# Kernel optimization log

Hardware: AMD Instinct MI355X
Metric: run time of the kernel (lower is better)

## Reference

```python
import jax, jax.numpy as jnp
import numpy as np
import math

NUM_HEADS = 8
HEAD_DIM = 32  # num_units 256 / 8 heads
TIME_DIM = 8
NEG_BIG = -2.0 ** 32 + 1.0


def _ffn(x, W1, b1, W2, b2):
    # two-layer relu MLP: 1 -> time_dim -> time_dim
    h = jax.nn.relu(x @ W1 + b1)
    return jax.nn.relu(h @ W2 + b2)


def _time_gsm_kernel(t, pW1, pb1, pW2, pb2, sW1, sb1, sW2, sb2, bW1, bb1, bW2, bb2):
    # t: [B, L] timestamps -> kernel [B, L, L]
    tt = t[..., None]  # [B, L, 1]
    period = _ffn(tt, pW1, pb1, pW2, pb2)        # [B, L, td]
    qpq = (2.0 * math.pi) * period * tt           # [B, L, td]
    period_diff = qpq[:, :, None, :] - qpq[:, None, :, :]  # [B, Lq, Lk, td]
    cos_enc = jnp.cos(period_diff)
    sigma = _ffn(tt, sW1, sb1, sW2, sb2)          # [B, L, td]
    sq = sigma[:, :, None, :] + 1e-6              # [B, Lq, 1, td] bcast
    sk = sigma[:, None, :, :] + 1e-6              # [B, 1, Lk, td] bcast
    denom = sq ** 2 + sk ** 2
    t_diff = t[:, :, None] - t[:, None, :]        # [B, Lq, Lk]
    exp_enc = jnp.exp(-(t_diff[..., None] ** 2) / denom)
    local_enc = jnp.sqrt(2.0 * sq * sk / denom)
    basis = _ffn(tt, bW1, bb1, bW2, bb2)          # [B, L, td]
    basis_qk = basis[:, :, None, :] * basis[:, None, :, :]
    return jnp.sum(basis_qk * local_enc * exp_enc * cos_enc, axis=-1)  # [B, L, L]


def setup_inputs() -> dict:
    key = jax.random.key(0)
    ks = jax.random.split(key, 20)
    B, L, U = 4, 1024, 256
    td = TIME_DIM
    inp = {
        'query_input': jax.random.normal(ks[0], (B, L, U), dtype=jnp.float32),
        'input_tensor': jax.random.normal(ks[1], (B, L, U), dtype=jnp.float32),
        'input_mask': jnp.ones((B, L), dtype=jnp.int32),
        'time_inputs': jax.random.uniform(ks[2], (B, L), dtype=jnp.float32) * 100.0,
        'att_bias': jnp.zeros((1,), dtype=jnp.int32),
        'Wq': jax.random.normal(ks[3], (U, U), dtype=jnp.float32) * 0.05,
        'Wk': jax.random.normal(ks[4], (U, U), dtype=jnp.float32) * 0.05,
        'Wv': jax.random.normal(ks[5], (U, U), dtype=jnp.float32) * 0.05,
    }
    names = ['p', 's', 'b']
    i = 6
    for n in names:
        inp[n + 'W1'] = jax.random.normal(ks[i], (1, td), dtype=jnp.float32) * 0.5; i += 1
        inp[n + 'b1'] = jnp.zeros((td,), dtype=jnp.float32)
        inp[n + 'W2'] = jax.random.normal(ks[i], (td, td), dtype=jnp.float32) * 0.5; i += 1
        inp[n + 'b2'] = jnp.zeros((td,), dtype=jnp.float32)
    return inp


def reference(query_input, input_tensor, input_mask, time_inputs, att_bias,
              Wq, Wk, Wv,
              pW1, pb1, pW2, pb2, sW1, sb1, sW2, sb2, bW1, bb1, bW2, bb2):
    B, Lq, U = query_input.shape
    Lk = input_tensor.shape[1]
    H, dh = NUM_HEADS, HEAD_DIM

    Q = (query_input @ Wq).reshape(B, Lq, H, dh).transpose(0, 2, 1, 3)  # [B,H,Lq,dh]
    K = (input_tensor @ Wk).reshape(B, Lk, H, dh).transpose(0, 2, 1, 3)
    V = (input_tensor @ Wv).reshape(B, Lk, H, dh).transpose(0, 2, 1, 3)

    scale = 1.0 / math.sqrt(dh)
    scores = jnp.einsum('bhqd,bhkd->bhqk', Q, K) * scale  # [B,H,Lq,Lk]

    tk = _time_gsm_kernel(time_inputs, pW1, pb1, pW2, pb2,
                          sW1, sb1, sW2, sb2, bW1, bb1, bW2, bb2)  # [B,Lq,Lk]
    scores = scores + tk[:, None, :, :] * scale

    # key padding mask: zero-norm keys get -inf-like score
    key_masks = jnp.sign(jnp.sum(jnp.abs(K), axis=-1))  # [B,H,Lk]
    scores = jnp.where(key_masks[:, :, None, :] == 0.0, NEG_BIG, scores)

    # direction == 'forward': allow strictly row > col (strict causal)
    idx = jnp.arange(Lk)
    causal = (idx[:, None] > idx[None, :]).astype(scores.dtype)  # [Lq,Lk]
    scores = scores + (1.0 - causal) * -10000.0

    attn = jax.nn.softmax(scores, axis=-1)

    query_masks = jnp.sign(jnp.sum(jnp.abs(Q), axis=-1))  # [B,H,Lq]
    attn = attn * query_masks[..., None]
    # dropout rate 0.0 -> identity

    out = jnp.einsum('bhqk,bhkd->bhqd', attn, V)
    out = out.transpose(0, 2, 1, 3).reshape(B, Lq, U)
    out = out * input_mask.astype(jnp.float32)[..., None]
    return out
```

## Files before the change

### kernel.cpp

```cpp
#include <hip/hip_runtime.h>
#include <math.h>

#define B_DIM 4
#define L_DIM 1024
#define H_DIM 8
#define D_DIM 32
#define TD 8
#define NTILES_TOT 1056
#define SCALE 0.17677669529663687f

typedef unsigned short ushort_t;
typedef __attribute__((ext_vector_type(8))) short short8v;
typedef __attribute__((ext_vector_type(4))) float f32x4;

__device__ __forceinline__ int ntiles_of(int qt) { return (qt >> 1) + 1; }
__device__ __forceinline__ int off_of(int qt) {
  int m = qt >> 1;
  return (qt & 1) ? (m + 1) * (m + 1) : m * m + m;
}
__device__ __forceinline__ void qcseg(int x, int& qc, int& s) {
  if (x < 4) { qc = x; s = 0; }
  else if (x < 12) { qc = 4 + ((x - 4) >> 1); s = (x - 4) & 1; }
  else if (x < 24) { int t = x - 12; qc = 8 + t / 3; s = t % 3; }
  else { int t = x - 24; qc = 12 + (t >> 2); s = t & 3; }
}

__device__ __forceinline__ ushort_t f2bf(float f) {
  unsigned u = __builtin_bit_cast(unsigned, f);
  u += 0x7FFFu + ((u >> 16) & 1u);
  return (ushort_t)(u >> 16);
}
__device__ __forceinline__ float bf2f(ushort_t h) {
  return __builtin_bit_cast(float, ((unsigned)h) << 16);
}
__device__ __forceinline__ short8v pack84(float4 a, float4 b) {
  short8v r;
  r[0] = (short)f2bf(a.x); r[1] = (short)f2bf(a.y);
  r[2] = (short)f2bf(a.z); r[3] = (short)f2bf(a.w);
  r[4] = (short)f2bf(b.x); r[5] = (short)f2bf(b.y);
  r[6] = (short)f2bf(b.z); r[7] = (short)f2bf(b.w);
  return r;
}

__global__ __launch_bounds__(256) void prep_kernel(
    const float* __restrict__ t_in,
    const float* __restrict__ pW1, const float* __restrict__ pb1,
    const float* __restrict__ pW2, const float* __restrict__ pb2,
    const float* __restrict__ sW1, const float* __restrict__ sb1,
    const float* __restrict__ sW2, const float* __restrict__ sb2,
    const float* __restrict__ bW1, const float* __restrict__ bb1,
    const float* __restrict__ bW2, const float* __restrict__ bb2,
    float* __restrict__ ptf, float* __restrict__ sg, float* __restrict__ bs,
    const float* __restrict__ Xq, const float* __restrict__ Xi,
    ushort_t* __restrict__ Xfq, ushort_t* __restrict__ Xfi,
    const float* __restrict__ Wq, const float* __restrict__ Wk,
    const float* __restrict__ Wv, ushort_t* __restrict__ Wf) {
  const int blk = blockIdx.x;
  const int tid = threadIdx.x;
  if (blk < 512) {
    const int lin = blk * 256 + tid;
    const int i = lin >> 5;
    const int slot = lin & 31;
    const int z = slot >> 3, e = slot & 7;
    if (z == 3) return;
    const float* W1 = (z == 0) ? pW1 : (z == 1) ? sW1 : bW1;
    const float* b1 = (z == 0) ? pb1 : (z == 1) ? sb1 : bb1;
    const float* W2 = (z == 0) ? pW2 : (z == 1) ? sW2 : bW2;
    const float* b2 = (z == 0) ? pb2 : (z == 1) ? sb2 : bb2;
    const double t = (double)t_in[i];
    double acc = (double)b2[e];
#pragma unroll
    for (int d = 0; d < 8; ++d) {
      double hv = t * (double)W1[d] + (double)b1[d];
      hv = hv > 0.0 ? hv : 0.0;
      acc += hv * (double)W2[d * 8 + e];
    }
    acc = acc > 0.0 ? acc : 0.0;
    const size_t o = (size_t)i * TD + e;
    if (z == 0) {
      double pt = acc * t;
      ptf[o] = (float)(pt - floor(pt));
    } else if (z == 1) {
      sg[o] = (float)(acc + 1e-6);
    } else {
      bs[o] = (float)acc;
    }
  } else if (blk < 1536) {
    const int xb = blk - 512;
    const float* X = (xb < 512) ? Xq : Xi;
    ushort_t* O = (xb < 512) ? Xfq : Xfi;
    const int lin = (xb & 511) * 256 + tid;
    const int row = lin >> 5, q = lin & 31;
    const float* src = &X[(size_t)row * 256 + q * 8];
    short8v f = pack84(*(const float4*)src, *(const float4*)(src + 4));
    size_t idx = ((size_t)((row >> 4) * 8 + (q >> 2)) * 64 + (q & 3) * 16 + (row & 15)) * 8;
    *(short8v*)&O[idx] = f;
  } else {
    const int wb = blk - 1536;
    const int z = wb >> 5;
    const float* W = (z == 0) ? Wq : (z == 1) ? Wk : Wv;
    const int lin = (wb & 31) * 256 + tid;
    const int kt = lin >> 10, g = (lin >> 8) & 3, n = lin & 255;
    short8v f;
#pragma unroll
    for (int i2 = 0; i2 < 8; ++i2)
      f[i2] = (short)f2bf(W[(size_t)(kt * 32 + g * 8 + i2) * 256 + n]);
    size_t idx = ((size_t)((z * 8 + kt) * 16 + (n >> 4)) * 64 + g * 16 + (n & 15)) * 8;
    *(short8v*)&Wf[idx] = f;
  }
}

__global__ __launch_bounds__(256) void work_kernel(
    const ushort_t* __restrict__ Xfq, const ushort_t* __restrict__ Xfi,
    const ushort_t* __restrict__ Wf,
    ushort_t* __restrict__ Qf, ushort_t* __restrict__ Kf,
    ushort_t* __restrict__ Vf,
    const float* __restrict__ ptf, const float* __restrict__ sg,
    const float* __restrict__ bs, const float* __restrict__ t_in,
    float* __restrict__ tkbuf) {
  __shared__ __align__(16) float ptq[16 * 8], qsh[16 * 8], qbh[16 * 8];
  __shared__ __align__(16) float ptk[32 * 12], ksh[32 * 12], kbh[32 * 12];
  __shared__ float trow[16], tcol[32];
  const int blk = blockIdx.x;
  const int tid = threadIdx.x;

  if (blk < 384) {
    const int z = blk >> 7;
    const int rem = blk & 127;
    const int m0t = (rem & 31) * 8;
    const int n0 = (rem >> 5) * 64;
    const ushort_t* Xf = (z == 0) ? Xfq : Xfi;
    const int w = tid >> 6, l = tid & 63, lg = l >> 4, lc = l & 15;
    const int wm = w >> 1, wn = w & 1;

    f32x4 acc[4][2];
#pragma unroll
    for (int mi = 0; mi < 4; ++mi)
#pragma unroll
      for (int ni = 0; ni < 2; ++ni) acc[mi][ni] = (f32x4){0.f, 0.f, 0.f, 0.f};

    for (int kt0 = 0; kt0 < 8; ++kt0) {
      short8v a[4], bfr[2];
#pragma unroll
      for (int mi = 0; mi < 4; ++mi)
        a[mi] = *(const short8v*)&Xf[((size_t)(m0t + wm * 4 + mi) * 8 + kt0) * 512 + l * 8];
#pragma unroll
      for (int ni = 0; ni < 2; ++ni)
        bfr[ni] = *(const short8v*)&Wf[((size_t)(z * 8 + kt0) * 16 + (n0 >> 4) + wn * 2 + ni) * 512 + l * 8];
#pragma unroll
      for (int mi = 0; mi < 4; ++mi)
#pragma unroll
        for (int ni = 0; ni < 2; ++ni)
          acc[mi][ni] = __builtin_amdgcn_mfma_f32_16x16x32_bf16(a[mi], bfr[ni], acc[mi][ni], 0, 0, 0);
    }

#pragma unroll
    for (int mi = 0; mi < 4; ++mi) {
#pragma unroll
      for (int ni = 0; ni < 2; ++ni) {
        const int col = n0 + wn * 32 + ni * 16 + lc;
        const int hh = col >> 5, d = col & 31;
#pragma unroll
        for (int r = 0; r < 4; ++r) {
          const int row = (m0t + wm * 4 + mi) * 16 + lg * 4 + r;
          const int bb = row >> 10, lr = row & (L_DIM - 1);
          float v = acc[mi][ni][r];
          if (z == 0) v *= SCALE;
          const ushort_t bv = f2bf(v);
          if (z == 2) {
            Vf[(((size_t)(bb * H_DIM + hh) * 32 + (lr >> 5)) * 2 + (d >> 4)) * 512 +
               (((lr >> 3) & 3) * 16 + (d & 15)) * 8 + (lr & 7)] = bv;
          } else {
            ushort_t* of16 = (z == 0) ? Qf : Kf;
            of16[((size_t)((bb * H_DIM + hh) * 64 + (lr >> 4))) * 512 +
                 ((d >> 3) * 16 + (lr & 15)) * 8 + (d & 7)] = bv;
          }
        }
      }
    }
  } else {
    const int lin = blk - 384;
    const int b = lin / NTILES_TOT;
    const int t1 = lin - b * NTILES_TOT;
    int m = (int)sqrtf((float)t1 + 1.0f);
    while (m * m + m > t1) --m;
    while ((m + 1) * (m + 1) + (m + 1) <= t1) ++m;
    const int rem = t1 - (m * m + m);
    int qt, kt;
    if (rem <= m) { qt = 2 * m; kt = rem; }
    else          { qt = 2 * m + 1; kt = rem - (m + 1); }
    const int q0 = qt << 4, k0 = kt << 5;

    if (tid < 16) trow[tid] = t_in[b * L_DIM + q0 + tid];
    if (tid < 32) tcol[tid] = t_in[b * L_DIM + k0 + tid];
    if (tid < 128) {
      const int i = tid >> 3, d = tid & 7;
      const size_t base = (size_t)(b * L_DIM + q0 + i) * TD + d;
      ptq[i * 8 + d] = ptf[base];
      qsh[i * 8 + d] = sg[base];
      qbh[i * 8 + d] = bs[base];
    }
    {
      const int j = tid >> 3, d = tid & 7;
      const size_t base = (size_t)(b * L_DIM + k0 + j) * TD + d;
      ptk[j * 12 + d] = ptf[base];
      ksh[j * 12 + d] = sg[base];
      kbh[j * 12 + d] = bs[base];
    }
    __syncthreads();

    const int r = tid & 3;
    const int lr2 = tid >> 2;
    const int i = ((lr2 >> 4) << 2) | r;
    float pq[8], qs_[8], qb_[8];
    *(float4*)&pq[0]  = *(const float4*)&ptq[i * 8];
    *(float4*)&pq[4]  = *(const float4*)&ptq[i * 8 + 4];
    *(float4*)&qs_[0] = *(const float4*)&qsh[i * 8];
    *(float4*)&qs_[4] = *(const float4*)&qsh[i * 8 + 4];
    *(float4*)&qb_[0] = *(const float4*)&qbh[i * 8];
    *(float4*)&qb_[4] = *(const float4*)&qbh[i * 8 + 4];
    const float ti = trow[i];

    float* dst = &tkbuf[(size_t)(b * NTILES_TOT + off_of(qt) + kt) * 512];
#pragma unroll
    for (int pp = 0; pp < 2; ++pp) {
      const int j = pp * 16 + (lr2 & 15);
      float td2 = ti - tcol[j];
      td2 *= td2;
      float pk[8], ks_[8], kb_[8];
      *(float4*)&pk[0]  = *(const float4*)&ptk[j * 12];
      *(float4*)&pk[4]  = *(const float4*)&ptk[j * 12 + 4];
      *(float4*)&ks_[0] = *(const float4*)&ksh[j * 12];
      *(float4*)&ks_[4] = *(const float4*)&ksh[j * 12 + 4];
      *(float4*)&kb_[0] = *(const float4*)&kbh[j * 12];
      *(float4*)&kb_[4] = *(const float4*)&kbh[j * 12 + 4];
      float a = 0.f;
#pragma unroll
      for (int d = 0; d < TD; ++d) {
        const float sqd = qs_[d], skd = ks_[d];
        const float denom = sqd * sqd + skd * skd;
        const float inv = __builtin_amdgcn_rcpf(denom);
        const float ee = __expf(-td2 * inv);
        const float le = __builtin_amdgcn_sqrtf(2.f * sqd * skd * inv);
        const float dq = __builtin_fabsf(pq[d] - pk[d]);
        const float ce = __builtin_amdgcn_cosf(dq);
        a += qb_[d] * kb_[d] * (le * ee * ce);
      }
      dst[tid + (pp << 8)] = a * SCALE;
    }
  }
}

__global__ __launch_bounds__(256, 4) void attn_partial_kernel(
    const ushort_t* __restrict__ Qf, const ushort_t* __restrict__ Kf,
    const ushort_t* __restrict__ Vf, const float* __restrict__ tkbuf,
    float* __restrict__ Opart, float* __restrict__ MLpart) {
  __shared__ __align__(16) ushort_t lds_p[4][1024];
  const int h = blockIdx.y;
  const int b = blockIdx.z;
  int qc, seg;
  qcseg((int)blockIdx.x, qc, seg);
  const int tid = threadIdx.x;
  const int w = tid >> 6;
  const int l = tid & 63;
  const int lg = l >> 4;
  const int lc = l & 15;
  const int qbase = qc * 64 + w * 16;
  const int qt = qbase >> 4;
  const int fb = (b * H_DIM + h) * 64;
  const int vb = (b * H_DIM + h) * 32;

  short8v qfrag = *(const short8v*)&Qf[((size_t)(fb + qt)) * 512 + l * 8];

  f32x4 O0 = {0.f, 0.f, 0.f, 0.f};
  f32x4 O1 = {0.f, 0.f, 0.f, 0.f};
  float mrow[4] = {-1e30f, -1e30f, -1e30f, -1e30f};
  float lrow[4] = {0.f, 0.f, 0.f, 0.f};
  const float* tk_qt = &tkbuf[(size_t)(b * NTILES_TOT + off_of(qt)) * 512];
  ushort_t* Pw = lds_p[w];

  const int kc0 = seg * 4;
  const int kc1 = (kc0 + 3 < qc) ? kc0 + 3 : qc;
  for (int kc = kc0; kc <= kc1; ++kc) {
    const bool diag = (kc == qc);
    const size_t kb_ = ((size_t)(fb + kc * 4)) * 512 + l * 8;
    short8v kf0 = *(const short8v*)&Kf[kb_];
    short8v kf1 = *(const short8v*)&Kf[kb_ + 512];
    short8v kf2 = *(const short8v*)&Kf[kb_ + 1024];
    short8v kf3 = *(const short8v*)&Kf[kb_ + 1536];
    const size_t tb_ = (size_t)(kc * 2) * 512 + l * 4;
    float4 t0 = *(const float4*)&tk_qt[tb_];
    float4 t1 = *(const float4*)&tk_qt[tb_ + 256];
    float4 t2 = *(const float4*)&tk_qt[tb_ + 512];
    float4 t3 = *(const float4*)&tk_qt[tb_ + 768];
    const size_t vb_ = ((size_t)(vb + kc * 2)) * 1024 + l * 8;
    short8v vf0 = *(const short8v*)&Vf[vb_];
    short8v vf1 = *(const short8v*)&Vf[vb_ + 512];
    short8v vf2 = *(const short8v*)&Vf[vb_ + 1024];
    short8v vf3 = *(const short8v*)&Vf[vb_ + 1536];

    f32x4 z4 = {0.f, 0.f, 0.f, 0.f};
    __builtin_amdgcn_s_setprio(1);
    f32x4 sv0 = __builtin_amdgcn_mfma_f32_16x16x32_bf16(qfrag, kf0, z4, 0, 0, 0);
    f32x4 sv1 = __builtin_amdgcn_mfma_f32_16x16x32_bf16(qfrag, kf1, z4, 0, 0, 0);
    f32x4 sv2 = __builtin_amdgcn_mfma_f32_16x16x32_bf16(qfrag, kf2, z4, 0, 0, 0);
    f32x4 sv3 = __builtin_amdgcn_mfma_f32_16x16x32_bf16(qfrag, kf3, z4, 0, 0, 0);
    __builtin_amdgcn_s_setprio(0);

    float s[4][4];
#pragma unroll
    for (int r = 0; r < 4; ++r) {
      s[0][r] = sv0[r] + (&t0.x)[r];
      s[1][r] = sv1[r] + (&t1.x)[r];
      s[2][r] = sv2[r] + (&t2.x)[r];
      s[3][r] = sv3[r] + (&t3.x)[r];
    }
    if (diag) {
#pragma unroll
      for (int kt = 0; kt < 4; ++kt) {
        const int col = kc * 64 + kt * 16 + lc;
#pragma unroll
        for (int r = 0; r < 4; ++r)
          if (col >= qbase + lg * 4 + r) s[kt][r] = -10000.0f;
      }
    }

#pragma unroll
    for (int r = 0; r < 4; ++r) {
      float tmax = fmaxf(fmaxf(s[0][r], s[1][r]), fmaxf(s[2][r], s[3][r]));
      tmax = fmaxf(tmax, __shfl_xor(tmax, 1));
      tmax = fmaxf(tmax, __shfl_xor(tmax, 2));
      tmax = fmaxf(tmax, __shfl_xor(tmax, 4));
      tmax = fmaxf(tmax, __shfl_xor(tmax, 8));
      float mnew = fmaxf(mrow[r], tmax);
      float cf = __expf(mrow[r] - mnew);
      mrow[r] = mnew;
      float p0 = __expf(s[0][r] - mnew);
      float p1 = __expf(s[1][r] - mnew);
      float p2 = __expf(s[2][r] - mnew);
      float p3 = __expf(s[3][r] - mnew);
      lrow[r] = lrow[r] * cf + ((p0 + p1) + (p2 + p3));
      O0[r] *= cf;
      O1[r] *= cf;
      const int pb = ((lc >> 3) << 7) + ((lg * 4 + r) << 3) + (lc & 7);
      Pw[pb] = f2bf(p0);
      Pw[pb + 256] = f2bf(p1);
      Pw[pb + 512] = f2bf(p2);
      Pw[pb + 768] = f2bf(p3);
    }
    short8v pf0 = *(const short8v*)&Pw[l * 8];
    short8v pf1 = *(const short8v*)&Pw[(64 + l) * 8];
    __builtin_amdgcn_s_setprio(1);
    O0 = __builtin_amdgcn_mfma_f32_16x16x32_bf16(pf0, vf0, O0, 0, 0, 0);
    O1 = __builtin_amdgcn_mfma_f32_16x16x32_bf16(pf0, vf1, O1, 0, 0, 0);
    O0 = __builtin_amdgcn_mfma_f32_16x16x32_bf16(pf1, vf2, O0, 0, 0, 0);
    O1 = __builtin_amdgcn_mfma_f32_16x16x32_bf16(pf1, vf3, O1, 0, 0, 0);
    __builtin_amdgcn_s_setprio(0);
  }

  const int pslot = (b * H_DIM + h) * 16 + qc;
  float* Ob = &Opart[(size_t)pslot * 8192 + seg * 2048];
  *(f32x4*)&Ob[tid * 8] = O0;
  *(f32x4*)&Ob[tid * 8 + 4] = O1;
  float* mlb = &MLpart[(size_t)pslot * 512 + seg * 128];
#pragma unroll
  for (int r = 0; r < 4; ++r) {
    float lr_ = lrow[r];
    lr_ += __shfl_xor(lr_, 1);
    lr_ += __shfl_xor(lr_, 2);
    lr_ += __shfl_xor(lr_, 4);
    lr_ += __shfl_xor(lr_, 8);
    if (lc == 0) {
      mlb[w * 16 + lg * 4 + r] = mrow[r];
      mlb[64 + w * 16 + lg * 4 + r] = lr_;
    }
  }
}

__global__ __launch_bounds__(256) void combine_row0_kernel(
    const ushort_t* __restrict__ Qf, const ushort_t* __restrict__ Kf,
    const ushort_t* __restrict__ Vf, const float* __restrict__ tkbuf,
    const float* __restrict__ Opart, const float* __restrict__ MLpart,
    const int* __restrict__ imask, float* __restrict__ out) {
  __shared__ float p_s[L_DIM];
  __shared__ float qsh[D_DIM];
  __shared__ float red[8][33];
  __shared__ float rtmp[4];
  const int h = blockIdx.y;
  const int b = blockIdx.z;
  const int tid = threadIdx.x;
  const int fb = (b * H_DIM + h) * 64;
  const int vb = (b * H_DIM + h) * 32;

  if (blockIdx.x == 16) {
    if (tid < D_DIM)
      qsh[tid] = bf2f(Qf[(size_t)fb * 512 + (tid >> 3) * 128 + (tid & 7)]);
    __syncthreads();
    float lmax = -1e30f;
    for (int j = tid; j < L_DIM; j += 256) {
      int i = j & 15;
      float tkv = tkbuf[(size_t)(b * NTILES_TOT + off_of(j >> 4)) * 512 +
                        (((i >> 2) << 6) | (i & 3))];
      const ushort_t* kp = &Kf[(size_t)(fb + (j >> 4)) * 512 + (j & 15) * 8];
      float dot = 0.f;
#pragma unroll
      for (int o = 0; o < 4; ++o) {
        short8v kv = *(const short8v*)&kp[o * 128];
#pragma unroll
        for (int u = 0; u < 8; ++u) dot += qsh[o * 8 + u] * bf2f((ushort_t)kv[u]);
      }
      float sc = dot + tkv;
      p_s[j] = sc;
      lmax = fmaxf(lmax, sc);
    }
#pragma unroll
    for (int o = 1; o < 64; o <<= 1) lmax = fmaxf(lmax, __shfl_xor(lmax, o));
    if ((tid & 63) == 0) rtmp[tid >> 6] = lmax;
    __syncthreads();
    const float bmax = fmaxf(fmaxf(rtmp[0], rtmp[1]), fmaxf(rtmp[2], rtmp[3]));
    __syncthreads();
    float lsumv = 0.f;
    for (int j = tid; j < L_DIM; j += 256) {
      float pv = __expf(p_s[j] - bmax);
      p_s[j] = pv;
      lsumv += pv;
    }
#pragma unroll
    for (int o = 1; o < 64; o <<= 1) lsumv += __shfl_xor(lsumv, o);
    if ((tid & 63) == 0) rtmp[tid >> 6] = lsumv;
    __syncthreads();
    const float bsum = rtmp[0] + rtmp[1] + rtmp[2] + rtmp[3];
    const int g = tid >> 5, d = tid & 31;
    float a = 0.f;
    for (int j = g * 128; j < g * 128 + 128; ++j) {
      float v = bf2f(Vf[(((size_t)(vb + (j >> 5))) * 2 + (d >> 4)) * 512 +
                        (((j >> 3) & 3) * 16 + (d & 15)) * 8 + (j & 7)]);
      a = fmaf(p_s[j], v, a);
    }
    red[g][d] = a;
    __syncthreads();
    if (tid < D_DIM) {
      float acc = 0.f;
#pragma unroll
      for (int gg = 0; gg < 8; ++gg) acc += red[gg][tid];
      float qabs = 0.f;
#pragma unroll
      for (int dd = 0; dd < D_DIM; ++dd) qabs += fabsf(qsh[dd]);
      const float qmv = qabs > 0.f ? 1.f : 0.f;
      out[((size_t)b * L_DIM) * 256 + h * D_DIM + tid] =
          acc * (1.0f / bsum) * qmv * (float)imask[b * L_DIM];
    }
    return;
  }

  const int qc = (int)blockIdx.x;
  const int nseg = (qc >> 2) + 1;
  const int w = tid >> 6;
  const int l = tid & 63;
  const int lg = l >> 4;
  const int lc = l & 15;
  const int qbase = qc * 64 + w * 16;
  const int qt = qbase >> 4;
  const int pslot = (b * H_DIM + h) * 16 + qc;
  const float* Ob = &Opart[(size_t)pslot * 8192];
  const float* mlb = &MLpart[(size_t)pslot * 512];

  short8v qfrag = *(const short8v*)&Qf[((size_t)(fb + qt)) * 512 + l * 8];
  float qabs_l = 0.f;
#pragma unroll
  for (int j = 0; j < 8; ++j) qabs_l += fabsf(bf2f((ushort_t)qfrag[j]));
  qabs_l += __shfl_xor(qabs_l, 16);
  qabs_l += __shfl_xor(qabs_l, 32);
  const float qm = (qabs_l > 0.f) ? 1.f : 0.f;

  float ms[4][4], ls[4][4];
#pragma unroll
  for (int s = 0; s < 4; ++s) {
    if (s < nseg) {
#pragma unroll
      for (int r = 0; r < 4; ++r) {
        ms[s][r] = mlb[s * 128 + w * 16 + lg * 4 + r];
        ls[s][r] = mlb[s * 128 + 64 + w * 16 + lg * 4 + r];
      }
    }
  }
  float M[4], L[4];
#pragma unroll
  for (int r = 0; r < 4; ++r) {
    float mm = ms[0][r];
#pragma unroll
    for (int s = 1; s < 4; ++s)
      if (s < nseg) mm = fmaxf(mm, ms[s][r]);
    M[r] = mm;
    L[r] = 0.f;
  }
  f32x4 O0 = {0.f, 0.f, 0.f, 0.f};
  f32x4 O1 = {0.f, 0.f, 0.f, 0.f};
#pragma unroll
  for (int s = 0; s < 4; ++s) {
    if (s < nseg) {
      f32x4 o0 = *(const f32x4*)&Ob[s * 2048 + tid * 8];
      f32x4 o1 = *(const f32x4*)&Ob[s * 2048 + tid * 8 + 4];
#pragma unroll
      for (int r = 0; r < 4; ++r) {
        const float f = __expf(ms[s][r] - M[r]);
        L[r] += ls[s][r] * f;
        O0[r] += o0[r] * f;
        O1[r] += o1[r] * f;
      }
    }
  }

#pragma unroll
  for (int r = 0; r < 4; ++r) {
    const int rr = lg * 4 + r;
    const int qrow = qbase + rr;
    float qmr = __shfl(qm, rr);
    float im = (float)imask[b * L_DIM + qrow];
    float scl = (1.0f / L[r]) * qmr * im;
    if (qrow != 0) {
      float* op = &out[((size_t)(b * L_DIM + qrow)) * 256 + h * D_DIM];
      op[lc] = O0[r] * scl;
      op[16 + lc] = O1[r] * scl;
    }
  }
}

extern "C" void kernel_launch(void* const* d_in, const int* in_sizes, int n_in,
                              void* d_out, int out_size, void* d_ws, size_t ws_size,
                              hipStream_t stream) {
  (void)in_sizes; (void)n_in; (void)out_size; (void)ws_size;
  const float* query = (const float*)d_in[0];
  const float* input = (const float*)d_in[1];
  const int* imask = (const int*)d_in[2];
  const float* t_in = (const float*)d_in[3];
  const float* Wq = (const float*)d_in[5];
  const float* Wk = (const float*)d_in[6];
  const float* Wv = (const float*)d_in[7];
  const float* pW1 = (const float*)d_in[8],  *pb1 = (const float*)d_in[9];
  const float* pW2 = (const float*)d_in[10], *pb2 = (const float*)d_in[11];
  const float* sW1 = (const float*)d_in[12], *sb1 = (const float*)d_in[13];
  const float* sW2 = (const float*)d_in[14], *sb2 = (const float*)d_in[15];
  const float* bW1 = (const float*)d_in[16], *bb1 = (const float*)d_in[17];
  const float* bW2 = (const float*)d_in[18], *bb2 = (const float*)d_in[19];
  float* out = (float*)d_out;

  const int M = B_DIM * L_DIM;
  char* p = (char*)d_ws;
  ushort_t* Qf = (ushort_t*)p;  p += (size_t)M * 256 * 2;
  ushort_t* Kf = (ushort_t*)p;  p += (size_t)M * 256 * 2;
  ushort_t* Vf = (ushort_t*)p;  p += (size_t)M * 256 * 2;
  ushort_t* Xfq = (ushort_t*)p; p += (size_t)M * 256 * 2;
  ushort_t* Xfi = (ushort_t*)p; p += (size_t)M * 256 * 2;
  ushort_t* Wfb = (ushort_t*)p; p += (size_t)3 * 256 * 256 * 2;
  float* ptf = (float*)p;       p += (size_t)M * TD * 4;
  float* sg = (float*)p;        p += (size_t)M * TD * 4;
  float* bs = (float*)p;        p += (size_t)M * TD * 4;
  float* tkbuf = (float*)p;     p += (size_t)B_DIM * NTILES_TOT * 512 * 4;
  float* Opart = (float*)p;     p += (size_t)512 * 8192 * 4;
  float* MLpart = (float*)p;

  prep_kernel<<<1632, 256, 0, stream>>>(
      t_in, pW1, pb1, pW2, pb2, sW1, sb1, sW2, sb2, bW1, bb1, bW2, bb2,
      ptf, sg, bs, query, input, Xfq, Xfi, Wq, Wk, Wv, Wfb);
  work_kernel<<<384 + B_DIM * NTILES_TOT, 256, 0, stream>>>(
      Xfq, Xfi, Wfb, Qf, Kf, Vf, ptf, sg, bs, t_in, tkbuf);
  attn_partial_kernel<<<dim3(40, H_DIM, B_DIM), 256, 0, stream>>>(
      Qf, Kf, Vf, tkbuf, Opart, MLpart);
  combine_row0_kernel<<<dim3(17, H_DIM, B_DIM), 256, 0, stream>>>(
      Qf, Kf, Vf, tkbuf, Opart, MLpart, imask, out);
}
```

Measured before the change: 60.69 us.

## Fold prep kernel into work kernel: convert inputs on the fly, recompute time MLPs per tile

Removes the separate prep launch. The projection GEMM blocks now read fp32 X directly and convert it to bf16 in registers, and they stage their W slice into shared memory with a bf16 swizzle. Time-kernel tiles recompute the three small MLPs for their 48 timestamps in double precision, using weights held in shared memory. This saves a launch and the round trip of intermediate buffers through global memory, but adds redundant weight conversion per block, redundant MLP work per tile, and uncoalesced-ish fp32 X loads inside the GEMM loop.

```diff
diff --git a/kernel.cpp b/kernel.cpp
--- a/kernel.cpp
+++ b/kernel.cpp
@@ -42,97 +42,49 @@
   return r;
 }
 
-__global__ __launch_bounds__(256) void prep_kernel(
-    const float* __restrict__ t_in,
+__global__ __launch_bounds__(256) void work_kernel(
+    const float* __restrict__ Xq, const float* __restrict__ Xi,
+    const float* __restrict__ Wq, const float* __restrict__ Wk,
+    const float* __restrict__ Wv, const float* __restrict__ t_in,
     const float* __restrict__ pW1, const float* __restrict__ pb1,
     const float* __restrict__ pW2, const float* __restrict__ pb2,
     const float* __restrict__ sW1, const float* __restrict__ sb1,
     const float* __restrict__ sW2, const float* __restrict__ sb2,
     const float* __restrict__ bW1, const float* __restrict__ bb1,
     const float* __restrict__ bW2, const float* __restrict__ bb2,
-    float* __restrict__ ptf, float* __restrict__ sg, float* __restrict__ bs,
-    const float* __restrict__ Xq, const float* __restrict__ Xi,
-    ushort_t* __restrict__ Xfq, ushort_t* __restrict__ Xfi,
-    const float* __restrict__ Wq, const float* __restrict__ Wk,
-    const float* __restrict__ Wv, ushort_t* __restrict__ Wf) {
-  const int blk = blockIdx.x;
-  const int tid = threadIdx.x;
-  if (blk < 512) {
-    const int lin = blk * 256 + tid;
-    const int i = lin >> 5;
-    const int slot = lin & 31;
-    const int z = slot >> 3, e = slot & 7;
-    if (z == 3) return;
-    const float* W1 = (z == 0) ? pW1 : (z == 1) ? sW1 : bW1;
-    const float* b1 = (z == 0) ? pb1 : (z == 1) ? sb1 : bb1;
-    const float* W2 = (z == 0) ? pW2 : (z == 1) ? sW2 : bW2;
-    const float* b2 = (z == 0) ? pb2 : (z == 1) ? sb2 : bb2;
-    const double t = (double)t_in[i];
-    double acc = (double)b2[e];
-#pragma unroll
-    for (int d = 0; d < 8; ++d) {
-      double hv = t * (double)W1[d] + (double)b1[d];
-      hv = hv > 0.0 ? hv : 0.0;
-      acc += hv * (double)W2[d * 8 + e];
-    }
-    acc = acc > 0.0 ? acc : 0.0;
-    const size_t o = (size_t)i * TD + e;
-    if (z == 0) {
-      double pt = acc * t;
-      ptf[o] = (float)(pt - floor(pt));
-    } else if (z == 1) {
-      sg[o] = (float)(acc + 1e-6);
-    } else {
-      bs[o] = (float)acc;
-    }
-  } else if (blk < 1536) {
-    const int xb = blk - 512;
-    const float* X = (xb < 512) ? Xq : Xi;
-    ushort_t* O = (xb < 512) ? Xfq : Xfi;
-    const int lin = (xb & 511) * 256 + tid;
-    const int row = lin >> 5, q = lin & 31;
-    const float* src = &X[(size_t)row * 256 + q * 8];
-    short8v f = pack84(*(const float4*)src, *(const float4*)(src + 4));
-    size_t idx = ((size_t)((row >> 4) * 8 + (q >> 2)) * 64 + (q & 3) * 16 + (row & 15)) * 8;
-    *(short8v*)&O[idx] = f;
-  } else {
-    const int wb = blk - 1536;
-    const int z = wb >> 5;
-    const float* W = (z == 0) ? Wq : (z == 1) ? Wk : Wv;
-    const int lin = (wb & 31) * 256 + tid;
-    const int kt = lin >> 10, g = (lin >> 8) & 3, n = lin & 255;
-    short8v f;
-#pragma unroll
-    for (int i2 = 0; i2 < 8; ++i2)
-      f[i2] = (short)f2bf(W[(size_t)(kt * 32 + g * 8 + i2) * 256 + n]);
-    size_t idx = ((size_t)((z * 8 + kt) * 16 + (n >> 4)) * 64 + g * 16 + (n & 15)) * 8;
-    *(short8v*)&Wf[idx] = f;
-  }
-}
-
-__global__ __launch_bounds__(256) void work_kernel(
-    const ushort_t* __restrict__ Xfq, const ushort_t* __restrict__ Xfi,
-    const ushort_t* __restrict__ Wf,
     ushort_t* __restrict__ Qf, ushort_t* __restrict__ Kf,
-    ushort_t* __restrict__ Vf,
-    const float* __restrict__ ptf, const float* __restrict__ sg,
-    const float* __restrict__ bs, const float* __restrict__ t_in,
-    float* __restrict__ tkbuf) {
-  __shared__ __align__(16) float ptq[16 * 8], qsh[16 * 8], qbh[16 * 8];
-  __shared__ __align__(16) float ptk[32 * 12], ksh[32 * 12], kbh[32 * 12];
-  __shared__ float trow[16], tcol[32];
+    ushort_t* __restrict__ Vf, float* __restrict__ tkbuf) {
+  __shared__ __align__(16) char smem[32768];
   const int blk = blockIdx.x;
   const int tid = threadIdx.x;
 
   if (blk < 384) {
     const int z = blk >> 7;
     const int rem = blk & 127;
-    const int m0t = (rem & 31) * 8;
+    const int m0 = (rem & 31) * 128;
     const int n0 = (rem >> 5) * 64;
-    const ushort_t* Xf = (z == 0) ? Xfq : Xfi;
+    const float* X = (z == 0) ? Xq : Xi;
+    const float* W = (z == 0) ? Wq : (z == 1) ? Wk : Wv;
+    ushort_t* wl = (ushort_t*)smem;
     const int w = tid >> 6, l = tid & 63, lg = l >> 4, lc = l & 15;
     const int wm = w >> 1, wn = w & 1;
 
+#pragma unroll
+    for (int i = 0; i < 16; ++i) {
+      const int f = i * 256 + tid;
+      const int k = f >> 4, nc = (f & 15) << 2;
+      float4 v4 = *(const float4*)&W[(size_t)k * 256 + n0 + nc];
+      float va[4] = {v4.x, v4.y, v4.z, v4.w};
+      const int kt = k >> 5, lg2 = (k >> 3) & 3, j = k & 7;
+#pragma unroll
+      for (int u = 0; u < 4; ++u) {
+        const int nl = nc + u;
+        wl[(size_t)(kt * 4 + (nl >> 4)) * 512 + (lg2 * 16 + (nl & 15)) * 8 + j] =
+            f2bf(va[u]);
+      }
+    }
+    __syncthreads();
+
     f32x4 acc[4][2];
 #pragma unroll
     for (int mi = 0; mi < 4; ++mi)
@@ -142,11 +94,13 @@
     for (int kt0 = 0; kt0 < 8; ++kt0) {
       short8v a[4], bfr[2];
 #pragma unroll
-      for (int mi = 0; mi < 4; ++mi)
-        a[mi] = *(const short8v*)&Xf[((size_t)(m0t + wm * 4 + mi) * 8 + kt0) * 512 + l * 8];
+      for (int mi = 0; mi < 4; ++mi) {
+        const float* xp = &X[(size_t)(m0 + (wm * 4 + mi) * 16 + lc) * 256 + kt0 * 32 + lg * 8];
+        a[mi] = pack84(*(const float4*)xp, *(const float4*)(xp + 4));
+      }
 #pragma unroll
       for (int ni = 0; ni < 2; ++ni)
-        bfr[ni] = *(const short8v*)&Wf[((size_t)(z * 8 + kt0) * 16 + (n0 >> 4) + wn * 2 + ni) * 512 + l * 8];
+        bfr[ni] = *(const short8v*)&wl[(size_t)(kt0 * 4 + wn * 2 + ni) * 512 + l * 8];
 #pragma unroll
       for (int mi = 0; mi < 4; ++mi)
 #pragma unroll
@@ -162,7 +116,7 @@
         const int hh = col >> 5, d = col & 31;
 #pragma unroll
         for (int r = 0; r < 4; ++r) {
-          const int row = (m0t + wm * 4 + mi) * 16 + lg * 4 + r;
+          const int row = m0 + (wm * 4 + mi) * 16 + lg * 4 + r;
           const int bb = row >> 10, lr = row & (L_DIM - 1);
           float v = acc[mi][ni][r];
           if (z == 0) v *= SCALE;
@@ -179,6 +133,16 @@
       }
     }
   } else {
+    float* lw  = (float*)smem;
+    float* ptq = (float*)(smem + 1088);
+    float* qsh = (float*)(smem + 1088 + 512);
+    float* qbh = (float*)(smem + 1088 + 1024);
+    float* ptk = (float*)(smem + 1088 + 1536);
+    float* ksh = (float*)(smem + 1088 + 3072);
+    float* kbh = (float*)(smem + 1088 + 4608);
+    float* trow = (float*)(smem + 1088 + 6144);
+    float* tcol = (float*)(smem + 1088 + 6208);
+
     const int lin = blk - 384;
     const int b = lin / NTILES_TOT;
     const int t1 = lin - b * NTILES_TOT;
@@ -191,21 +155,44 @@
     else          { qt = 2 * m + 1; kt = rem - (m + 1); }
     const int q0 = qt << 4, k0 = kt << 5;
 
+    for (int s2 = tid; s2 < 264; s2 += 256) {
+      const int z = s2 / 88, o = s2 - z * 88;
+      const float* W1 = (z == 0) ? pW1 : (z == 1) ? sW1 : bW1;
+      const float* b1 = (z == 0) ? pb1 : (z == 1) ? sb1 : bb1;
+      const float* W2 = (z == 0) ? pW2 : (z == 1) ? sW2 : bW2;
+      const float* b2 = (z == 0) ? pb2 : (z == 1) ? sb2 : bb2;
+      float v;
+      if (o < 8) v = W1[o];
+      else if (o < 16) v = b1[o - 8];
+      else if (o < 80) v = W2[o - 16];
+      else v = b2[o - 80];
+      lw[s2] = v;
+    }
     if (tid < 16) trow[tid] = t_in[b * L_DIM + q0 + tid];
     if (tid < 32) tcol[tid] = t_in[b * L_DIM + k0 + tid];
-    if (tid < 128) {
-      const int i = tid >> 3, d = tid & 7;
-      const size_t base = (size_t)(b * L_DIM + q0 + i) * TD + d;
-      ptq[i * 8 + d] = ptf[base];
-      qsh[i * 8 + d] = sg[base];
-      qbh[i * 8 + d] = bs[base];
-    }
-    {
-      const int j = tid >> 3, d = tid & 7;
-      const size_t base = (size_t)(b * L_DIM + k0 + j) * TD + d;
-      ptk[j * 12 + d] = ptf[base];
-      ksh[j * 12 + d] = sg[base];
-      kbh[j * 12 + d] = bs[base];
+    __syncthreads();
+
+    for (int s = tid; s < 1152; s += 256) {
+      const int z = s / 384;
+      const int rm = s - z * 384;
+      const int p = rm >> 3, e = rm & 7;
+      const int gi = (p < 16) ? (q0 + p) : (k0 + p - 16);
+      const double t = (double)t_in[b * L_DIM + gi];
+      const float* wb = &lw[z * 88];
+      double acc = (double)wb[80 + e];
+#pragma unroll
+      for (int d = 0; d < 8; ++d) {
+        double hv = t * (double)wb[d] + (double)wb[8 + d];
+        hv = hv > 0.0 ? hv : 0.0;
+        acc += hv * (double)wb[16 + d * 8 + e];
+      }
+      acc = acc > 0.0 ? acc : 0.0;
+      float val;
+      if (z == 0) { double pt = acc * t; val = (float)(pt - floor(pt)); }
+      else if (z == 1) val = (float)(acc + 1e-6);
+      else val = (float)acc;
+      if (p < 16) (z == 0 ? ptq : z == 1 ? qsh : qbh)[p * 8 + e] = val;
+      else        (z == 0 ? ptk : z == 1 ? ksh : kbh)[(p - 16) * 12 + e] = val;
     }
     __syncthreads();
 
@@ -550,21 +537,14 @@
   ushort_t* Qf = (ushort_t*)p;  p += (size_t)M * 256 * 2;
   ushort_t* Kf = (ushort_t*)p;  p += (size_t)M * 256 * 2;
   ushort_t* Vf = (ushort_t*)p;  p += (size_t)M * 256 * 2;
-  ushort_t* Xfq = (ushort_t*)p; p += (size_t)M * 256 * 2;
-  ushort_t* Xfi = (ushort_t*)p; p += (size_t)M * 256 * 2;
-  ushort_t* Wfb = (ushort_t*)p; p += (size_t)3 * 256 * 256 * 2;
-  float* ptf = (float*)p;       p += (size_t)M * TD * 4;
-  float* sg = (float*)p;        p += (size_t)M * TD * 4;
-  float* bs = (float*)p;        p += (size_t)M * TD * 4;
   float* tkbuf = (float*)p;     p += (size_t)B_DIM * NTILES_TOT * 512 * 4;
   float* Opart = (float*)p;     p += (size_t)512 * 8192 * 4;
   float* MLpart = (float*)p;
 
-  prep_kernel<<<1632, 256, 0, stream>>>(
-      t_in, pW1, pb1, pW2, pb2, sW1, sb1, sW2, sb2, bW1, bb1, bW2, bb2,
-      ptf, sg, bs, query, input, Xfq, Xfi, Wq, Wk, Wv, Wfb);
   work_kernel<<<384 + B_DIM * NTILES_TOT, 256, 0, stream>>>(
-      Xfq, Xfi, Wfb, Qf, Kf, Vf, ptf, sg, bs, t_in, tkbuf);
+      query, input, Wq, Wk, Wv, t_in,
+      pW1, pb1, pW2, pb2, sW1, sb1, sW2, sb2, bW1, bb1, bW2, bb2,
+      Qf, Kf, Vf, tkbuf);
   attn_partial_kernel<<<dim3(40, H_DIM, B_DIM), 256, 0, stream>>>(
       Qf, Kf, Vf, tkbuf, Opart, MLpart);
   combine_row0_kernel<<<dim3(17, H_DIM, B_DIM), 256, 0, stream>>>(
```

Result: slower. 74.87 us (+23.4%).
